# Performance work log

Measured on AMD Instinct MI355X. Metric: run time of the kernel, lower is better.

Reference implementation:

```python
import jax, jax.numpy as jnp
import numpy as np

NUM_BITS = 8
PACKET = 1024
LENGTH = 8192
VDD = 1.0
VR = VDD / 2 ** NUM_BITS   # Vr = Vdd / 2**q_bits
VREF = VR
DELTA = 1e-30
W_SIZE = NUM_BITS * (NUM_BITS + 1) // 2  # 36


def setup_inputs() -> dict:
    key = jax.random.key(0)
    kx, kw = jax.random.split(key)
    x = jax.random.uniform(kx, (LENGTH, PACKET), dtype=jnp.float32)
    W = jax.random.normal(kw, (W_SIZE,), dtype=jnp.float32)
    return {"x": x, "W": W}


def reference(x, W):
    # Bit-serial SAR ADC recurrence. noisy_inference=False -> W_noisy = W.
    nb = NUM_BITS
    Qbits = [None] * nb          # each [length, packet]
    m = W.shape[0] - 1
    for j in reversed(range(nb)):
        bit_sum = W[m] * VREF    # scalar, broadcasts over [length, packet]
        m -= 1
        for k in range(j + 1, nb):
            bit_sum = bit_sum + (Qbits[k] + 1.0) * 0.5 * W[m] * VR
            m -= 1
        Qbits[j] = jnp.sign(x - bit_sum + DELTA)
    Q = jnp.stack(Qbits, axis=-1)                 # [length, packet, num_bits]
    # q = sum_b (Q_b + 1)/2 * Vr * 2^b
    scales = VR * (2.0 ** jnp.arange(nb, dtype=jnp.float32))  # [num_bits]
    q = jnp.einsum('lpb,b->lp', (Q + 1.0) * 0.5, scales)
    return (q.astype(jnp.float32), Q.astype(jnp.float32), W)
```

## Files before the change

kernel.cpp:

```cpp
#include <hip/hip_runtime.h>


constexpr int NB     = 8;
constexpr int TOTAL  = 8192 * 1024;
constexpr int NVEC   = TOTAL / 4;
constexpr int Q_OFF  = TOTAL;
constexpr int W_OFF  = TOTAL * (NB + 1);
constexpr float VRC  = 1.0f / 256.0f;

__global__ __launch_bounds__(256) void sar_adc_kernel(
    const float* __restrict__ x,
    const float* __restrict__ W,
    float* __restrict__ out)
{
    float w[36];
#pragma unroll
    for (int i = 0; i < 36; ++i) w[i] = W[i];

    if (blockIdx.x == 0 && threadIdx.x < 36) {
        out[W_OFF + threadIdx.x] = w[threadIdx.x];
    }

    const float4* __restrict__ x4 = (const float4*)x;
    float4* __restrict__ q4 = (float4*)out;
    float4* __restrict__ Q4 = (float4*)(out + Q_OFF);

    const int stride = gridDim.x * blockDim.x;
    for (int v = blockIdx.x * blockDim.x + threadIdx.x; v < NVEC; v += stride) {
        const float4 xv = x4[v];
        const float xe[4] = {xv.x, xv.y, xv.z, xv.w};
        float qout[4];
        float Qb[4][NB];

#pragma unroll
        for (int e = 0; e < 4; ++e) {
            const float xs = xe[e] * 256.0f;
            bool bit[NB];
            int m = 35;
#pragma unroll
            for (int j = NB - 1; j >= 0; --j) {
                float bs = w[m]; m--;
#pragma unroll
                for (int k = j + 1; k < NB; ++k) {
                    bs += bit[k] ? w[m] : 0.0f;
                    m--;
                }
                bit[j] = (xs - bs) >= 0.0f;
            }
            int n = 0;
#pragma unroll
            for (int b = 0; b < NB; ++b) {
                Qb[e][b] = bit[b] ? 1.0f : -1.0f;
                n += bit[b] ? (1 << b) : 0;
            }
            qout[e] = (float)n * VRC;
        }

        q4[v] = make_float4(qout[0], qout[1], qout[2], qout[3]);
#pragma unroll
        for (int t = 0; t < 8; ++t) {
            const int e = t >> 1;
            const int b0 = (t & 1) * 4;
            Q4[(size_t)v * 8 + t] =
                make_float4(Qb[e][b0 + 0], Qb[e][b0 + 1], Qb[e][b0 + 2], Qb[e][b0 + 3]);
        }
    }
}

extern "C" void kernel_launch(void* const* d_in, const int* in_sizes, int n_in,
                              void* d_out, int out_size, void* d_ws, size_t ws_size,
                              hipStream_t stream) {
    const float* x = (const float*)d_in[0];
    const float* W = (const float*)d_in[1];
    float* out = (float*)d_out;

    const int block = 256;
    const int grid = 2048;
    sar_adc_kernel<<<grid, block, 0, stream>>>(x, W, out);
}
```

Before: 158.7 us.

## Stage Q output through swizzled LDS for coalesced stores, one tile per block

Replaces the grid-stride loop with one 1024-element tile per block (8192 blocks). The per-thread Q bit vectors are written into a swizzled shared-memory buffer and then stored to global memory so that consecutive threads write consecutive float4s. The aim is to turn the strided 8-float4-per-thread stores into fully coalesced stores. It adds a __syncthreads, 32KB of LDS per block, and the cost of launching many more blocks.

```diff
diff --git a/kernel.cpp b/kernel.cpp
--- a/kernel.cpp
+++ b/kernel.cpp
@@ -3,16 +3,19 @@
 
 constexpr int NB     = 8;
 constexpr int TOTAL  = 8192 * 1024;
-constexpr int NVEC   = TOTAL / 4;
 constexpr int Q_OFF  = TOTAL;
 constexpr int W_OFF  = TOTAL * (NB + 1);
 constexpr float VRC  = 1.0f / 256.0f;
+constexpr int ELEMS_PER_BLOCK = 1024;
+constexpr int NBLOCKS = TOTAL / ELEMS_PER_BLOCK;
 
 __global__ __launch_bounds__(256) void sar_adc_kernel(
     const float* __restrict__ x,
     const float* __restrict__ W,
     float* __restrict__ out)
 {
+    __shared__ float4 lds[2048];
+
     float w[36];
 #pragma unroll
     for (int i = 0; i < 36; ++i) w[i] = W[i];
@@ -25,45 +28,58 @@
     float4* __restrict__ q4 = (float4*)out;
     float4* __restrict__ Q4 = (float4*)(out + Q_OFF);
 
-    const int stride = gridDim.x * blockDim.x;
-    for (int v = blockIdx.x * blockDim.x + threadIdx.x; v < NVEC; v += stride) {
-        const float4 xv = x4[v];
-        const float xe[4] = {xv.x, xv.y, xv.z, xv.w};
-        float qout[4];
-        float Qb[4][NB];
+    const int t    = threadIdx.x;
+    const int tile = blockIdx.x;
+    const int vin  = tile * 256 + t;
+
+    const float4 xv = x4[vin];
+    const float xe[4] = {xv.x, xv.y, xv.z, xv.w};
+    float qout[4];
+    float Qb[4][NB];
 
 #pragma unroll
-        for (int e = 0; e < 4; ++e) {
-            const float xs = xe[e] * 256.0f;
-            bool bit[NB];
-            int m = 35;
+    for (int e = 0; e < 4; ++e) {
+        const float xs = xe[e] * 256.0f;
+        bool bit[NB];
+        int m = 35;
 #pragma unroll
-            for (int j = NB - 1; j >= 0; --j) {
-                float bs = w[m]; m--;
+        for (int j = NB - 1; j >= 0; --j) {
+            float bs = w[m]; m--;
 #pragma unroll
-                for (int k = j + 1; k < NB; ++k) {
-                    bs += bit[k] ? w[m] : 0.0f;
-                    m--;
-                }
-                bit[j] = (xs - bs) >= 0.0f;
+            for (int k = j + 1; k < NB; ++k) {
+                bs += bit[k] ? w[m] : 0.0f;
+                m--;
             }
-            int n = 0;
+            bit[j] = (xs - bs) >= 0.0f;
+        }
+        int n = 0;
 #pragma unroll
-            for (int b = 0; b < NB; ++b) {
-                Qb[e][b] = bit[b] ? 1.0f : -1.0f;
-                n += bit[b] ? (1 << b) : 0;
-            }
-            qout[e] = (float)n * VRC;
+        for (int b = 0; b < NB; ++b) {
+            Qb[e][b] = bit[b] ? 1.0f : -1.0f;
+            n += bit[b] ? (1 << b) : 0;
         }
+        qout[e] = (float)n * VRC;
+    }
 
-        q4[v] = make_float4(qout[0], qout[1], qout[2], qout[3]);
+    q4[vin] = make_float4(qout[0], qout[1], qout[2], qout[3]);
+
 #pragma unroll
-        for (int t = 0; t < 8; ++t) {
-            const int e = t >> 1;
-            const int b0 = (t & 1) * 4;
-            Q4[(size_t)v * 8 + t] =
-                make_float4(Qb[e][b0 + 0], Qb[e][b0 + 1], Qb[e][b0 + 2], Qb[e][b0 + 3]);
-        }
+    for (int i = 0; i < 8; ++i) {
+        const int e  = i >> 1;
+        const int b0 = (i & 1) * 4;
+        lds[t * 8 + (i ^ (t & 7))] =
+            make_float4(Qb[e][b0 + 0], Qb[e][b0 + 1], Qb[e][b0 + 2], Qb[e][b0 + 3]);
+    }
+
+    __syncthreads();
+
+    const int qbase = tile * 2048;
+#pragma unroll
+    for (int s = 0; s < 8; ++s) {
+        const int f   = s * 256 + t;
+        const int tw  = f >> 3;
+        const int iw  = f & 7;
+        Q4[qbase + f] = lds[tw * 8 + (iw ^ (tw & 7))];
     }
 }
 
@@ -74,7 +90,5 @@
     const float* W = (const float*)d_in[1];
     float* out = (float*)d_out;
 
-    const int block = 256;
-    const int grid = 2048;
-    sar_adc_kernel<<<grid, block, 0, stream>>>(x, W, out);
+    sar_adc_kernel<<<NBLOCKS, 256, 0, stream>>>(x, W, out);
 }
```

New measurement: 167.8 us. +5.7%, slower.
